# Performance work log

Hardware: AMD Instinct MI355X
Metric: run time of the kernel (lower is better)

The kernel has to match this reference:

```python
import jax, jax.numpy as jnp
import numpy as np

LN_EPS = 1e-5


def setup_inputs() -> dict:
    key = jax.random.key(0)
    ks = jax.random.split(key, 4)
    B, N, C, K = 512, 100, 256, 3
    query = jax.random.normal(ks[0], (B, N, C), dtype=jnp.float32)
    value = jax.random.normal(ks[1], (B, N, C), dtype=jnp.float32)
    # nn.Linear(C, N+K): weight stored as [out,in] in torch; here use [in,out]
    W_wl = jax.random.normal(ks[2], (C, N + K), dtype=jnp.float32) / np.sqrt(C)
    b_wl = jax.random.normal(ks[3], (N + K,), dtype=jnp.float32) * 0.01
    ln_gamma = jnp.ones((C,), dtype=jnp.float32)
    ln_beta = jnp.zeros((C,), dtype=jnp.float32)
    return {"query": query, "value": value, "W_wl": W_wl, "b_wl": b_wl,
            "ln_gamma": ln_gamma, "ln_beta": ln_beta}


def reference(query, value, W_wl, b_wl, ln_gamma, ln_beta):
    B, N, C = query.shape
    K = W_wl.shape[1] - N
    # dynamic conv weights from query: [B, N, K] depthwise + [B, N, N] pointwise
    dy = jnp.einsum('bnc,ck->bnk', query, W_wl) + b_wl
    dw = dy[:, :, :K]          # depthwise kernels, one per (b, proposal)
    pw = dy[:, :, K:]          # pointwise mixing matrix [B, N, N]
    # depthwise conv1d along C with 'same' padding (cross-correlation like torch)
    pad_l = (K - 1) // 2
    pad_r = K - 1 - pad_l
    vp = jnp.pad(value, ((0, 0), (0, 0), (pad_l, pad_r)))
    depth = jnp.zeros_like(value)
    for k in range(K):  # K is tiny (3): static unrolled loop
        depth = depth + dw[:, :, k:k + 1] * vp[:, :, k:k + C]
    depth = jax.nn.relu(depth)
    # pointwise conv (kernel size 1) == per-sample NxN mix over proposals
    out = jnp.einsum('bnm,bmc->bnc', pw, depth)
    # LayerNorm over C
    mu = jnp.mean(out, axis=-1, keepdims=True)
    var = jnp.var(out, axis=-1, keepdims=True)
    out = (out - mu) * jax.lax.rsqrt(var + LN_EPS) * ln_gamma + ln_beta
    return out
```

## Files before the change

kernel.cpp:

```cpp
#include <hip/hip_runtime.h>

#define NN 100
#define CC 256
#define NKK 103
#define LDPW 136
#define OTS 260

typedef __bf16 bf16;
typedef __bf16 bf16x4 __attribute__((ext_vector_type(4)));
typedef __bf16 bf16x8 __attribute__((ext_vector_type(8)));
typedef float f32x4 __attribute__((ext_vector_type(4)));

__global__ void wl_transpose(const float* __restrict__ W, bf16* __restrict__ Wt)
{
    int idx = blockIdx.x * 256 + threadIdx.x;
    if (idx < NKK * CC) {
        int ka = idx >> 8;
        int k  = idx & 255;
        Wt[ka * CC + k] = (bf16)W[k * NKK + ka];
    }
}

__global__ __launch_bounds__(512, 4)
void dysepconv_fused(const float* __restrict__ query,
                     const float* __restrict__ value,
                     const bf16*  __restrict__ Wt,
                     const float* __restrict__ bwl,
                     const float* __restrict__ gamma,
                     const float* __restrict__ beta,
                     float* __restrict__ out)
{
    __shared__ __align__(16) char SMEM[52800];
    bf16*  PW = (bf16*)SMEM;
    float (*DW)[3]     = (float(*)[3])(SMEM + 27200);
    float (*RP)[NN][2] = (float(*)[NN][2])(SMEM + 28400);
    float (*RS)[2]     = (float(*)[2])(SMEM + 52000);
    float* OT = (float*)SMEM;

    const int t    = threadIdx.x;
    const int w    = t >> 6;
    const int lane = t & 63;
    const int ln16 = lane & 15;
    const int g    = lane >> 4;
    const int hi8  = g * 8;
    const int b    = blockIdx.x;
    const int cb   = w * 16 + ln16;

    const float* qb = query + (size_t)b * NN * CC;
    const float* vb = value + (size_t)b * NN * CC;

    f32x4 acc1[7];
    #pragma unroll
    for (int J = 0; J < 7; ++J) acc1[J] = (f32x4){0.f, 0.f, 0.f, 0.f};

    if (w < 7) {
        const int qrow = (w * 16 + ln16 < NN) ? (w * 16 + ln16) : (NN - 1);
        const float* qr = qb + qrow * CC;
        #pragma unroll
        for (int kc = 0; kc < 4; ++kc) {
            bf16x8 qf[2];
            #pragma unroll
            for (int s = 0; s < 2; ++s) {
                f32x4 a0 = *(const f32x4*)(qr + kc * 64 + s * 32 + hi8);
                f32x4 a1 = *(const f32x4*)(qr + kc * 64 + s * 32 + hi8 + 4);
                #pragma unroll
                for (int i = 0; i < 4; ++i) { qf[s][i] = (bf16)a0[i]; qf[s][i + 4] = (bf16)a1[i]; }
            }
            #pragma unroll
            for (int J = 0; J < 7; ++J) {
                const int rB = (J * 16 + ln16 < NKK) ? (J * 16 + ln16) : (NKK - 1);
                bf16x8 bv0 = *(const bf16x8*)(Wt + rB * CC + kc * 64 + hi8);
                bf16x8 bv1 = *(const bf16x8*)(Wt + rB * CC + kc * 64 + 32 + hi8);
                acc1[J] = __builtin_amdgcn_mfma_f32_16x16x32_bf16(qf[0], bv0, acc1[J], 0, 0, 0);
                acc1[J] = __builtin_amdgcn_mfma_f32_16x16x32_bf16(qf[1], bv1, acc1[J], 0, 0, 0);
                if (J == 3) __builtin_amdgcn_sched_barrier(0);
            }
        }
    }

    for (int i = t; i < NN * 28; i += 512) {
        int r = i / 28, m = 100 + (i - (i / 28) * 28);
        PW[r * LDPW + m] = (bf16)0.f;
    }
    float xv[8], yv[8];
    #pragma unroll
    for (int j = 0; j < 8; ++j) {
        int m = hi8 + j;
        const float* vr = vb + m * CC;
        xv[j] = vr[cb];
        yv[j] = vr[cb + 128];
    }
    if (w < 7) {
        #pragma unroll
        for (int J = 0; J < 7; ++J) {
            int kap = J * 16 + ln16;
            float bw = (kap < NKK) ? bwl[kap] : 0.f;
            #pragma unroll
            for (int r = 0; r < 4; ++r) {
                int n = w * 16 + g * 4 + r;
                if (n < NN && kap < NKK) {
                    float v = acc1[J][r] + bw;
                    if (kap < 3) DW[n][kap] = v;
                    else         PW[n * LDPW + (kap - 3)] = (bf16)v;
                }
            }
        }
    }
    __syncthreads();

    f32x4 acc2[2][7];
    #pragma unroll
    for (int st = 0; st < 2; ++st)
        #pragma unroll
        for (int I = 0; I < 7; ++I) acc2[st][I] = (f32x4){0.f, 0.f, 0.f, 0.f};

    #pragma unroll
    for (int ks = 0; ks < 4; ++ks) {
        if (ks) {
            #pragma unroll
            for (int j = 0; j < 8; ++j) {
                int m = ks * 32 + hi8 + j;
                bool mv = (m < NN);
                const float* vr = vb + m * CC;
                xv[j] = mv ? vr[cb]       : 0.f;
                yv[j] = mv ? vr[cb + 128] : 0.f;
            }
        }
        bf16x8 dv0, dv1;
        #pragma unroll
        for (int j = 0; j < 8; ++j) {
            int  m  = ks * 32 + hi8 + j;
            bool mv = (m < NN);
            int  mc = mv ? m : (NN - 1);
            float w0 = DW[mc][0], w1 = DW[mc][1], w2 = DW[mc][2];
            float x0 = xv[j], y0 = yv[j];
            float xm = __shfl(x0, (lane - 1) & 63), xp = __shfl(x0, (lane + 1) & 63);
            float ym = __shfl(y0, (lane - 1) & 63), yp = __shfl(y0, (lane + 1) & 63);
            if (ln16 == 0) {
                xm = (mv && cb > 0) ? vb[m * CC + cb - 1] : 0.f;
                ym = mv ? vb[m * CC + cb + 127] : 0.f;
            }
            if (ln16 == 15) {
                xp = mv ? vb[m * CC + cb + 1] : 0.f;
                yp = (mv && cb + 129 < CC) ? vb[m * CC + cb + 129] : 0.f;
            }
            float d0 = w0 * xm + w1 * x0 + w2 * xp;
            float d1 = w0 * ym + w1 * y0 + w2 * yp;
            dv0[j] = (bf16)(mv ? fmaxf(d0, 0.f) : 0.f);
            dv1[j] = (bf16)(mv ? fmaxf(d1, 0.f) : 0.f);
            if (j == 3) __builtin_amdgcn_sched_barrier(0);
        }
        #pragma unroll
        for (int I = 0; I < 7; ++I) {
            int row = I * 16 + ln16;
            row = (row < NN) ? row : (NN - 1);
            bf16x8 af = *(const bf16x8*)&PW[row * LDPW + ks * 32 + hi8];
            acc2[0][I] = __builtin_amdgcn_mfma_f32_16x16x32_bf16(af, dv0, acc2[0][I], 0, 0, 0);
            acc2[1][I] = __builtin_amdgcn_mfma_f32_16x16x32_bf16(af, dv1, acc2[1][I], 0, 0, 0);
            if (I == 3) __builtin_amdgcn_sched_barrier(0);
        }
    }

    const float gm0 = gamma[cb], gm1 = gamma[cb + 128];
    const float bt0 = beta[cb],  bt1 = beta[cb + 128];

    #pragma unroll
    for (int I = 0; I < 7; ++I) {
        #pragma unroll
        for (int r = 0; r < 4; ++r) {
            float a = acc2[0][I][r], e = acc2[1][I][r];
            float s1 = a + e, s2 = a * a + e * e;
            #pragma unroll
            for (int mk = 1; mk < 16; mk <<= 1) {
                s1 += __shfl_xor(s1, mk);
                s2 += __shfl_xor(s2, mk);
            }
            int n = I * 16 + g * 4 + r;
            if (ln16 == 0 && n < NN) {
                RP[w][n][0] = s1;
                RP[w][n][1] = s2;
            }
        }
    }
    __syncthreads();
    if (t < NN) {
        float S1 = 0.f, S2 = 0.f;
        #pragma unroll
        for (int wi = 0; wi < 8; ++wi) { S1 += RP[wi][t][0]; S2 += RP[wi][t][1]; }
        float mu  = S1 * (1.f / 256.f);
        float var = S2 * (1.f / 256.f) - mu * mu;
        RS[t][0] = mu;
        RS[t][1] = rsqrtf(fmaxf(var, 0.f) + 1e-5f);
    }
    __syncthreads();

    float* ob = out + (size_t)b * NN * CC;
    #pragma unroll
    for (int h = 0; h < 2; ++h) {
        const int n0 = h * 50;
        #pragma unroll
        for (int I = 0; I < 7; ++I) {
            #pragma unroll
            for (int r = 0; r < 4; ++r) {
                int n = I * 16 + g * 4 + r;
                if (n >= n0 && n < n0 + 50 && n < NN) {
                    float mu = RS[n][0], rs = RS[n][1];
                    int rt = n - n0;
                    OT[rt * OTS + cb]       = (acc2[0][I][r] - mu) * rs * gm0 + bt0;
                    OT[rt * OTS + cb + 128] = (acc2[1][I][r] - mu) * rs * gm1 + bt1;
                }
            }
        }
        __syncthreads();
        #pragma unroll
        for (int p = 0; p < 7; ++p) {
            int idx = p * 512 + t;
            if (idx < 50 * 64) {
                int row = idx >> 6, c4 = (idx & 63) << 2;
                *(f32x4*)(ob + (size_t)(n0 + row) * CC + c4) = *(const f32x4*)&OT[row * OTS + c4];
            }
        }
        if (h == 0) __syncthreads();
    }
}

extern "C" void kernel_launch(void* const* d_in, const int* in_sizes, int n_in,
                              void* d_out, int out_size, void* d_ws, size_t ws_size,
                              hipStream_t stream) {
    const float* query = (const float*)d_in[0];
    const float* value = (const float*)d_in[1];
    const float* W     = (const float*)d_in[2];
    const float* bwl   = (const float*)d_in[3];
    const float* gamma = (const float*)d_in[4];
    const float* beta  = (const float*)d_in[5];
    bf16* Wt = (bf16*)d_ws;

    wl_transpose<<<dim3((NKK * CC + 255) / 256), dim3(256), 0, stream>>>(W, Wt);
    dysepconv_fused<<<dim3(512), dim3(512), 0, stream>>>(query, value, Wt, bwl, gamma, beta, (float*)d_out);
}
```

Before: 195.6 us.

## Halve block to 256 threads with four column strips per wave

Each block now runs four waves instead of eight. Each wave computes two row tiles of the query GEMM and four 16-column strips of the pointwise GEMM, so more accumulators live in registers per thread. The PW fragment loaded from LDS is reused across four MFMAs instead of two, and each block has fewer waves to synchronise. The cost is higher register pressure (launch bounds 256,2) and less parallelism per block, which may lower the number of resident waves.

```diff
diff --git a/kernel.cpp b/kernel.cpp
--- a/kernel.cpp
+++ b/kernel.cpp
@@ -7,7 +7,6 @@
 #define OTS 260
 
 typedef __bf16 bf16;
-typedef __bf16 bf16x4 __attribute__((ext_vector_type(4)));
 typedef __bf16 bf16x8 __attribute__((ext_vector_type(8)));
 typedef float f32x4 __attribute__((ext_vector_type(4)));
 
@@ -21,7 +20,7 @@
     }
 }
 
-__global__ __launch_bounds__(512, 4)
+__global__ __launch_bounds__(256, 2)
 void dysepconv_fused(const float* __restrict__ query,
                      const float* __restrict__ value,
                      const bf16*  __restrict__ Wt,
@@ -44,132 +43,140 @@
     const int g    = lane >> 4;
     const int hi8  = g * 8;
     const int b    = blockIdx.x;
-    const int cb   = w * 16 + ln16;
+    const int cb0  = w * 16 + ln16;
 
     const float* qb = query + (size_t)b * NN * CC;
     const float* vb = value + (size_t)b * NN * CC;
 
-    f32x4 acc1[7];
-    #pragma unroll
-    for (int J = 0; J < 7; ++J) acc1[J] = (f32x4){0.f, 0.f, 0.f, 0.f};
-
-    if (w < 7) {
-        const int qrow = (w * 16 + ln16 < NN) ? (w * 16 + ln16) : (NN - 1);
-        const float* qr = qb + qrow * CC;
-        #pragma unroll
-        for (int kc = 0; kc < 4; ++kc) {
-            bf16x8 qf[2];
-            #pragma unroll
-            for (int s = 0; s < 2; ++s) {
-                f32x4 a0 = *(const f32x4*)(qr + kc * 64 + s * 32 + hi8);
-                f32x4 a1 = *(const f32x4*)(qr + kc * 64 + s * 32 + hi8 + 4);
-                #pragma unroll
-                for (int i = 0; i < 4; ++i) { qf[s][i] = (bf16)a0[i]; qf[s][i + 4] = (bf16)a1[i]; }
-            }
-            #pragma unroll
-            for (int J = 0; J < 7; ++J) {
-                const int rB = (J * 16 + ln16 < NKK) ? (J * 16 + ln16) : (NKK - 1);
-                bf16x8 bv0 = *(const bf16x8*)(Wt + rB * CC + kc * 64 + hi8);
-                bf16x8 bv1 = *(const bf16x8*)(Wt + rB * CC + kc * 64 + 32 + hi8);
-                acc1[J] = __builtin_amdgcn_mfma_f32_16x16x32_bf16(qf[0], bv0, acc1[J], 0, 0, 0);
-                acc1[J] = __builtin_amdgcn_mfma_f32_16x16x32_bf16(qf[1], bv1, acc1[J], 0, 0, 0);
-                if (J == 3) __builtin_amdgcn_sched_barrier(0);
-            }
-        }
-    }
-
-    for (int i = t; i < NN * 28; i += 512) {
+    f32x4 acc1[2][7];
+    #pragma unroll
+    for (int u = 0; u < 2; ++u)
+        #pragma unroll
+        for (int J = 0; J < 7; ++J) acc1[u][J] = (f32x4){0.f, 0.f, 0.f, 0.f};
+
+    #pragma unroll
+    for (int u = 0; u < 2; ++u) {
+        if (u == 0 || w < 3) {
+            const int tile = w + u * 4;
+            const int qrow = (tile * 16 + ln16 < NN) ? (tile * 16 + ln16) : (NN - 1);
+            const float* qr = qb + qrow * CC;
+            #pragma unroll
+            for (int kc = 0; kc < 4; ++kc) {
+                bf16x8 qf[2];
+                #pragma unroll
+                for (int s = 0; s < 2; ++s) {
+                    f32x4 a0 = *(const f32x4*)(qr + kc * 64 + s * 32 + hi8);
+                    f32x4 a1 = *(const f32x4*)(qr + kc * 64 + s * 32 + hi8 + 4);
+                    #pragma unroll
+                    for (int i = 0; i < 4; ++i) { qf[s][i] = (bf16)a0[i]; qf[s][i + 4] = (bf16)a1[i]; }
+                }
+                #pragma unroll
+                for (int J = 0; J < 7; ++J) {
+                    const int rB = (J * 16 + ln16 < NKK) ? (J * 16 + ln16) : (NKK - 1);
+                    bf16x8 bv0 = *(const bf16x8*)(Wt + rB * CC + kc * 64 + hi8);
+                    bf16x8 bv1 = *(const bf16x8*)(Wt + rB * CC + kc * 64 + 32 + hi8);
+                    acc1[u][J] = __builtin_amdgcn_mfma_f32_16x16x32_bf16(qf[0], bv0, acc1[u][J], 0, 0, 0);
+                    acc1[u][J] = __builtin_amdgcn_mfma_f32_16x16x32_bf16(qf[1], bv1, acc1[u][J], 0, 0, 0);
+                }
+            }
+        }
+    }
+
+    for (int i = t; i < NN * 28; i += 256) {
         int r = i / 28, m = 100 + (i - (i / 28) * 28);
         PW[r * LDPW + m] = (bf16)0.f;
     }
-    float xv[8], yv[8];
-    #pragma unroll
-    for (int j = 0; j < 8; ++j) {
-        int m = hi8 + j;
-        const float* vr = vb + m * CC;
-        xv[j] = vr[cb];
-        yv[j] = vr[cb + 128];
-    }
-    if (w < 7) {
-        #pragma unroll
-        for (int J = 0; J < 7; ++J) {
-            int kap = J * 16 + ln16;
-            float bw = (kap < NKK) ? bwl[kap] : 0.f;
-            #pragma unroll
-            for (int r = 0; r < 4; ++r) {
-                int n = w * 16 + g * 4 + r;
-                if (n < NN && kap < NKK) {
-                    float v = acc1[J][r] + bw;
-                    if (kap < 3) DW[n][kap] = v;
-                    else         PW[n * LDPW + (kap - 3)] = (bf16)v;
+    float xv[4][8];
+    #pragma unroll
+    for (int s = 0; s < 4; ++s)
+        #pragma unroll
+        for (int j = 0; j < 8; ++j) {
+            int m = hi8 + j;
+            xv[s][j] = vb[m * CC + cb0 + 64 * s];
+        }
+    #pragma unroll
+    for (int u = 0; u < 2; ++u) {
+        if (u == 0 || w < 3) {
+            #pragma unroll
+            for (int J = 0; J < 7; ++J) {
+                int kap = J * 16 + ln16;
+                float bw = (kap < NKK) ? bwl[kap] : 0.f;
+                #pragma unroll
+                for (int r = 0; r < 4; ++r) {
+                    int n = (w + u * 4) * 16 + g * 4 + r;
+                    if (n < NN && kap < NKK) {
+                        float v = acc1[u][J][r] + bw;
+                        if (kap < 3) DW[n][kap] = v;
+                        else         PW[n * LDPW + (kap - 3)] = (bf16)v;
+                    }
                 }
             }
         }
     }
     __syncthreads();
 
-    f32x4 acc2[2][7];
-    #pragma unroll
-    for (int st = 0; st < 2; ++st)
-        #pragma unroll
-        for (int I = 0; I < 7; ++I) acc2[st][I] = (f32x4){0.f, 0.f, 0.f, 0.f};
+    f32x4 acc2[4][7];
+    #pragma unroll
+    for (int s = 0; s < 4; ++s)
+        #pragma unroll
+        for (int I = 0; I < 7; ++I) acc2[s][I] = (f32x4){0.f, 0.f, 0.f, 0.f};
 
     #pragma unroll
     for (int ks = 0; ks < 4; ++ks) {
         if (ks) {
             #pragma unroll
-            for (int j = 0; j < 8; ++j) {
-                int m = ks * 32 + hi8 + j;
-                bool mv = (m < NN);
-                const float* vr = vb + m * CC;
-                xv[j] = mv ? vr[cb]       : 0.f;
-                yv[j] = mv ? vr[cb + 128] : 0.f;
-            }
-        }
-        bf16x8 dv0, dv1;
+            for (int s = 0; s < 4; ++s)
+                #pragma unroll
+                for (int j = 0; j < 8; ++j) {
+                    int m = ks * 32 + hi8 + j;
+                    bool mv = (m < NN);
+                    xv[s][j] = mv ? vb[m * CC + cb0 + 64 * s] : 0.f;
+                }
+        }
+        bf16x8 dv[4];
         #pragma unroll
         for (int j = 0; j < 8; ++j) {
             int  m  = ks * 32 + hi8 + j;
             bool mv = (m < NN);
             int  mc = mv ? m : (NN - 1);
             float w0 = DW[mc][0], w1 = DW[mc][1], w2 = DW[mc][2];
-            float x0 = xv[j], y0 = yv[j];
-            float xm = __shfl(x0, (lane - 1) & 63), xp = __shfl(x0, (lane + 1) & 63);
-            float ym = __shfl(y0, (lane - 1) & 63), yp = __shfl(y0, (lane + 1) & 63);
-            if (ln16 == 0) {
-                xm = (mv && cb > 0) ? vb[m * CC + cb - 1] : 0.f;
-                ym = mv ? vb[m * CC + cb + 127] : 0.f;
-            }
-            if (ln16 == 15) {
-                xp = mv ? vb[m * CC + cb + 1] : 0.f;
-                yp = (mv && cb + 129 < CC) ? vb[m * CC + cb + 129] : 0.f;
-            }
-            float d0 = w0 * xm + w1 * x0 + w2 * xp;
-            float d1 = w0 * ym + w1 * y0 + w2 * yp;
-            dv0[j] = (bf16)(mv ? fmaxf(d0, 0.f) : 0.f);
-            dv1[j] = (bf16)(mv ? fmaxf(d1, 0.f) : 0.f);
-            if (j == 3) __builtin_amdgcn_sched_barrier(0);
+            #pragma unroll
+            for (int s = 0; s < 4; ++s) {
+                int c = cb0 + 64 * s;
+                float x0 = xv[s][j];
+                float xm = __shfl(x0, (lane - 1) & 63);
+                float xp = __shfl(x0, (lane + 1) & 63);
+                if (ln16 == 0)  xm = (mv && c > 0)      ? vb[m * CC + c - 1] : 0.f;
+                if (ln16 == 15) xp = (mv && c + 1 < CC) ? vb[m * CC + c + 1] : 0.f;
+                float d = w0 * xm + w1 * x0 + w2 * xp;
+                dv[s][j] = (bf16)(mv ? fmaxf(d, 0.f) : 0.f);
+            }
         }
         #pragma unroll
         for (int I = 0; I < 7; ++I) {
             int row = I * 16 + ln16;
             row = (row < NN) ? row : (NN - 1);
             bf16x8 af = *(const bf16x8*)&PW[row * LDPW + ks * 32 + hi8];
-            acc2[0][I] = __builtin_amdgcn_mfma_f32_16x16x32_bf16(af, dv0, acc2[0][I], 0, 0, 0);
-            acc2[1][I] = __builtin_amdgcn_mfma_f32_16x16x32_bf16(af, dv1, acc2[1][I], 0, 0, 0);
-            if (I == 3) __builtin_amdgcn_sched_barrier(0);
-        }
-    }
-
-    const float gm0 = gamma[cb], gm1 = gamma[cb + 128];
-    const float bt0 = beta[cb],  bt1 = beta[cb + 128];
+            #pragma unroll
+            for (int s = 0; s < 4; ++s)
+                acc2[s][I] = __builtin_amdgcn_mfma_f32_16x16x32_bf16(af, dv[s], acc2[s][I], 0, 0, 0);
+        }
+    }
+
+    float gm[4], bt[4];
+    #pragma unroll
+    for (int s = 0; s < 4; ++s) { gm[s] = gamma[cb0 + 64 * s]; bt[s] = beta[cb0 + 64 * s]; }
 
     #pragma unroll
     for (int I = 0; I < 7; ++I) {
         #pragma unroll
         for (int r = 0; r < 4; ++r) {
-            float a = acc2[0][I][r], e = acc2[1][I][r];
-            float s1 = a + e, s2 = a * a + e * e;
+            float s1 = 0.f, s2 = 0.f;
+            #pragma unroll
+            for (int s = 0; s < 4; ++s) {
+                float a = acc2[s][I][r];
+                s1 += a; s2 += a * a;
+            }
             #pragma unroll
             for (int mk = 1; mk < 16; mk <<= 1) {
                 s1 += __shfl_xor(s1, mk);
@@ -186,7 +193,7 @@
     if (t < NN) {
         float S1 = 0.f, S2 = 0.f;
         #pragma unroll
-        for (int wi = 0; wi < 8; ++wi) { S1 += RP[wi][t][0]; S2 += RP[wi][t][1]; }
+        for (int wi = 0; wi < 4; ++wi) { S1 += RP[wi][t][0]; S2 += RP[wi][t][1]; }
         float mu  = S1 * (1.f / 256.f);
         float var = S2 * (1.f / 256.f) - mu * mu;
         RS[t][0] = mu;
@@ -206,15 +213,16 @@
                 if (n >= n0 && n < n0 + 50 && n < NN) {
                     float mu = RS[n][0], rs = RS[n][1];
                     int rt = n - n0;
-                    OT[rt * OTS + cb]       = (acc2[0][I][r] - mu) * rs * gm0 + bt0;
-                    OT[rt * OTS + cb + 128] = (acc2[1][I][r] - mu) * rs * gm1 + bt1;
+                    #pragma unroll
+                    for (int s = 0; s < 4; ++s)
+                        OT[rt * OTS + cb0 + 64 * s] = (acc2[s][I][r] - mu) * rs * gm[s] + bt[s];
                 }
             }
         }
         __syncthreads();
         #pragma unroll
-        for (int p = 0; p < 7; ++p) {
-            int idx = p * 512 + t;
+        for (int p = 0; p < 13; ++p) {
+            int idx = p * 256 + t;
             if (idx < 50 * 64) {
                 int row = idx >> 6, c4 = (idx & 63) << 2;
                 *(f32x4*)(ob + (size_t)(n0 + row) * CC + c4) = *(const f32x4*)&OT[row * OTS + c4];
@@ -236,5 +244,5 @@
     bf16* Wt = (bf16*)d_ws;
 
     wl_transpose<<<dim3((NKK * CC + 255) / 256), dim3(256), 0, stream>>>(W, Wt);
-    dysepconv_fused<<<dim3(512), dim3(512), 0, stream>>>(query, value, Wt, bwl, gamma, beta, (float*)d_out);
+    dysepconv_fused<<<dim3(512), dim3(256), 0, stream>>>(query, value, Wt, bwl, gamma, beta, (float*)d_out);
 }
```

New measurement: 184.5 us. 5.7% less time.
